# Kernel tuning notes

Measured on AMD Instinct MI355X. Metric: run time of the kernel, lower is better.

The kernel has to match this reference:

```python
import jax, jax.numpy as jnp
import numpy as np

NEG_SLOPE = 0.2


def setup_inputs() -> dict:
    key = jax.random.key(0)
    k1, k2, k3 = jax.random.split(key, 3)
    bs, n_agents, input_dim = 32, 512, 128
    n_heads, hidden_dim = 8, 64
    h = jax.random.normal(k1, (bs, n_agents, input_dim), dtype=jnp.float32)
    # Linear(input_dim, n_heads*hidden_dim, bias=False), stored as [in, out]
    W = jax.random.normal(k2, (input_dim, n_heads * hidden_dim), dtype=jnp.float32) * (1.0 / np.sqrt(input_dim))
    # xavier_uniform with gain=1.414 on shape (1, n_heads, 2*hidden_dim)
    fan = n_heads + 2 * hidden_dim
    bound = 1.414 * np.sqrt(6.0 / fan)
    att_a = jax.random.uniform(k3, (1, n_heads, 2 * hidden_dim), dtype=jnp.float32,
                               minval=-bound, maxval=bound)
    return {"h": h, "W": W, "att_a": att_a}


def reference(h, W, att_a):
    bs, n_agents, _ = h.shape
    n_heads = att_a.shape[1]
    hidden_dim = att_a.shape[2] // 2
    # h_prime: [bs, n_heads, n_agents, hidden_dim]
    h_prime = (h @ W).reshape(bs, n_agents, n_heads, hidden_dim).transpose(0, 2, 1, 3)
    # Additive score decomposes exactly: (a1.h_i + a2.h_j) == sum(cat(h_i,h_j)*a)
    a_src = att_a[0, :, :hidden_dim]   # [n_heads, hidden_dim]
    a_dst = att_a[0, :, hidden_dim:]   # [n_heads, hidden_dim]
    e_src = jnp.einsum('bhnd,hd->bhn', h_prime, a_src)  # score contribution of node i (row)
    e_dst = jnp.einsum('bhnd,hd->bhn', h_prime, a_dst)  # contribution of node j (col)
    e = e_src[:, :, :, None] + e_dst[:, :, None, :]     # [bs, n_heads, n, n]
    e = jnp.where(e >= 0, e, NEG_SLOPE * e)             # leaky_relu(0.2)
    attention = jax.nn.softmax(e, axis=-1)
    h_new = jnp.einsum('bhnm,bhmd->bhnd', attention, h_prime)
    return jax.nn.elu(h_new)
```

## Files before the change

kernel.cpp:

```cpp
#include <hip/hip_runtime.h>

#define BS 32
#define NA 512
#define ID 128
#define NH 8
#define HD 64
#define NHD 512
#define NEG 0.2f
#define NC 32
#define CH 16
#define NW 8

__global__ __launch_bounds__(256) void k1_gemm(
    const float* __restrict__ h, const float* __restrict__ W,
    float* __restrict__ hp) {
  int blk = blockIdx.x;
  int b = blk >> 5;
  int n0 = (blk & 31) * 16;
  int t = threadIdx.x;
  int lane = t & 63, w = t >> 6;
  int r0 = __builtin_amdgcn_readfirstlane((w >> 1) * 8);
  int chalf = __builtin_amdgcn_readfirstlane(w & 1);
  int col = chalf * 256 + lane * 4;
  int head = col >> 6;
  int d0 = col & 63;
  const float* arow = h + ((size_t)b * NA + n0 + r0) * ID;
  const float* wptr = W + col;

  float4 a0c = {0,0,0,0}, a1c = {0,0,0,0}, a2c = {0,0,0,0}, a3c = {0,0,0,0};
  float4 a4c = {0,0,0,0}, a5c = {0,0,0,0}, a6c = {0,0,0,0}, a7c = {0,0,0,0};

#define K1_ROW(I, C, KK)                                                      \
  { float a_ = arow[(I) * ID + kc + (KK)];                                    \
    C.x += a_ * wv.x; C.y += a_ * wv.y; C.z += a_ * wv.z; C.w += a_ * wv.w; }
  #pragma unroll 1
  for (int kc = 0; kc < ID; kc += 8) {
    #pragma unroll
    for (int kk = 0; kk < 8; ++kk) {
      float4 wv = *(const float4*)(wptr + (size_t)(kc + kk) * NHD);
      K1_ROW(0, a0c, kk) K1_ROW(1, a1c, kk) K1_ROW(2, a2c, kk)
      K1_ROW(3, a3c, kk) K1_ROW(4, a4c, kk) K1_ROW(5, a5c, kk)
      K1_ROW(6, a6c, kk) K1_ROW(7, a7c, kk)
    }
  }
#undef K1_ROW
  size_t off = ((((size_t)b * NH + head) * NA) + (n0 + r0)) * HD + d0;
  *(float4*)(hp + off) = a0c; off += HD;
  *(float4*)(hp + off) = a1c; off += HD;
  *(float4*)(hp + off) = a2c; off += HD;
  *(float4*)(hp + off) = a3c; off += HD;
  *(float4*)(hp + off) = a4c; off += HD;
  *(float4*)(hp + off) = a5c; off += HD;
  *(float4*)(hp + off) = a6c; off += HD;
  *(float4*)(hp + off) = a7c;
}

__global__ __launch_bounds__(512, 2) void k2_fused(
    const float* __restrict__ att, float* __restrict__ io) {
  __shared__ float tv[NA]; __shared__ int tpm[NA];
  __shared__ float sv[NA]; __shared__ int spm[NA];
  __shared__ float wp[NA]; __shared__ float wn[NA];
  __shared__ float rawP8[NW * 64]; __shared__ float rawN8[NW * 64];
  __shared__ float sufPc[(NW + 1) * 64]; __shared__ float preNc[(NW + 1) * 64];
  __shared__ float zps[NA + 1]; __shared__ float znp[NA + 1];
  __shared__ float szP[NC]; __shared__ float szN[NC];
  __shared__ float sufZ[NC + 1]; __shared__ float preZ[NC + 1];
  __shared__ float4 abi[NA];
  __shared__ int jsr[NA];
  __shared__ int Earr[NA];
  __shared__ float asrc[HD]; __shared__ float adst[HD];

  int bh = blockIdx.x;
  int head = bh & (NH - 1);
  int t = threadIdx.x;
  int lane = t & 63, w = t >> 6;
  float* vbase = io + (size_t)bh * NA * HD;

  if (t < 2 * HD) {
    float a = att[head * 2 * HD + t];
    if (t < HD) asrc[t] = a; else adst[t - HD] = a;
  }
  __syncthreads();

  float vt, vs; int it = t, is_ = t;
  {
    const float4* vr = (const float4*)(vbase + (size_t)t * HD);
    float s0 = 0.f, s1 = 0.f, t0 = 0.f, t1 = 0.f;
    #pragma unroll
    for (int j = 0; j < HD / 4; j += 2) {
      float4 v0 = vr[j], v1 = vr[j + 1];
      s0 += v0.x*asrc[4*j+0] + v0.y*asrc[4*j+1] + v0.z*asrc[4*j+2] + v0.w*asrc[4*j+3];
      t0 += v0.x*adst[4*j+0] + v0.y*adst[4*j+1] + v0.z*adst[4*j+2] + v0.w*adst[4*j+3];
      s1 += v1.x*asrc[4*j+4] + v1.y*asrc[4*j+5] + v1.z*asrc[4*j+6] + v1.w*asrc[4*j+7];
      t1 += v1.x*adst[4*j+4] + v1.y*adst[4*j+5] + v1.z*adst[4*j+6] + v1.w*adst[4*j+7];
    }
    vs = s0 + s1; vt = t0 + t1;
  }

  for (int size = 2; size <= NA; size <<= 1) {
    bool dirAsc = ((t & size) == 0);
    for (int stride = size >> 1; stride > 0; stride >>= 1) {
      float pt, ps; int pit, pis;
      if (stride >= 64) {
        tv[t] = vt; tpm[t] = it; sv[t] = vs; spm[t] = is_;
        __syncthreads();
        pt = tv[t ^ stride]; pit = tpm[t ^ stride];
        ps = sv[t ^ stride]; pis = spm[t ^ stride];
        __syncthreads();
      } else {
        pt = __shfl_xor(vt, stride, 64); pit = __shfl_xor(it, stride, 64);
        ps = __shfl_xor(vs, stride, 64); pis = __shfl_xor(is_, stride, 64);
      }
      bool mn = (((t & stride) == 0) == dirAsc);
      if (mn ? (pt < vt) : (pt > vt)) { vt = pt; it = pit; }
      if (mn ? (ps < vs) : (ps > vs)) { vs = ps; is_ = pis; }
    }
  }
  tv[t] = vt; tpm[t] = it; sv[t] = vs; spm[t] = is_;
  __syncthreads();

  float cmax = fmaxf(tv[NA - 1], 0.f);
  float amax = fmaxf(sv[NA - 1], 0.f);
  wp[t] = __expf(vt - cmax);
  wn[t] = __expf(NEG * vt - cmax);
  __syncthreads();

  float vreg[64];
  {
    float aP = 0.f, aN = 0.f;
    #pragma unroll
    for (int jj = 0; jj < 64; ++jj) {
      int j = (w << 6) + jj;
      float vv = vbase[(size_t)tpm[j] * HD + lane];
      vreg[jj] = vv;
      aP += wp[j] * vv;
      aN += wn[j] * vv;
    }
    rawP8[(w << 6) + lane] = aP;
    rawN8[(w << 6) + lane] = aN;
  }
  __syncthreads();

  if (t < 64) {
    int d = t; float run = 0.f;
    sufPc[NW * 64 + d] = 0.f;
    for (int ww = NW - 1; ww >= 0; --ww) {
      run += rawP8[ww * 64 + d]; sufPc[ww * 64 + d] = run;
    }
  } else if (t < 128) {
    int d = t - 64; float run = 0.f;
    for (int ww = 0; ww <= NW; ++ww) {
      preNc[ww * 64 + d] = run;
      if (ww < NW) run += rawN8[ww * 64 + d];
    }
  } else if (t < 160) {
    int c = t - 128; float a = 0.f;
    for (int j = c * CH; j < c * CH + CH; ++j) a += wp[j];
    szP[c] = a;
  } else if (t < 192) {
    int c = t - 160; float a = 0.f;
    for (int j = c * CH; j < c * CH + CH; ++j) a += wn[j];
    szN[c] = a;
  }
  __syncthreads();

  if (t == 0) {
    float run = 0.f; sufZ[NC] = 0.f;
    for (int cc = NC - 1; cc >= 0; --cc) { run += szP[cc]; sufZ[cc] = run; }
  } else if (t == 1) {
    float run = 0.f;
    for (int cc = 0; cc <= NC; ++cc) { preZ[cc] = run; if (cc < NC) run += szN[cc]; }
  }
  __syncthreads();

  {
    int ch = t >> 4;
    float a = 0.f;
    for (int k = t; k < ch * CH + CH; ++k) a += wp[k];
    zps[t] = a + sufZ[ch + 1];
    float b2 = 0.f;
    for (int k = ch * CH; k < t; ++k) b2 += wn[k];
    znp[t] = preZ[ch] + b2;
    if (t == 0) { zps[NA] = 0.f; znp[NA] = preZ[NC]; }
  }
  __syncthreads();

  {
    float A = __expf(vs - amax);
    float B = __expf(NEG * vs - amax);
    float key = -vs;
    int lo = 0, hi = NA;
    while (lo < hi) { int mid = (lo + hi) >> 1; if (tv[mid] < key) lo = mid + 1; else hi = mid; }
    float den = A * zps[lo] + B * znp[lo];
    float4 q; q.x = A; q.y = B; q.z = 1.f / den; q.w = __int_as_float(is_);
    abi[t] = q;
    jsr[t] = lo;
  }
  __syncthreads();

  {
    int lo = 0, hi = NA;
    while (lo < hi) { int mid = (lo + hi) >> 1; if (jsr[mid] > t) lo = mid + 1; else hi = mid; }
    Earr[t] = lo;
  }
  __syncthreads();

  {
    float sufPv = sufPc[w * 64 + lane];
    float preSeedN = preNc[w * 64 + lane];
    float runN = 0.f;
    size_t obase = (size_t)bh * NA * HD + lane;
    int eprev = (w == 0) ? NA : Earr[(w << 6) - 1];
    #pragma unroll
    for (int jj = 0; jj < 64; ++jj) {
      int j = (w << 6) + jj;
      int ecur = Earr[j];
      float preNv = preSeedN + runN;
      for (int r = ecur; r < eprev; ++r) {
        float4 q = abi[r];
        float x = (q.x * sufPv + q.y * preNv) * q.z;
        int orow = __float_as_int(q.w);
        io[obase + (size_t)orow * HD] = x > 0.f ? x : __expf(x) - 1.f;
      }
      float vv = vreg[jj];
      sufPv -= wp[j] * vv;
      runN  += wn[j] * vv;
      eprev = ecur;
    }
    if (w == NW - 1) {
      float preNv = preSeedN + runN;
      for (int r = 0; r < eprev; ++r) {
        float4 q = abi[r];
        float x = (q.y * preNv) * q.z;
        int orow = __float_as_int(q.w);
        io[obase + (size_t)orow * HD] = x > 0.f ? x : __expf(x) - 1.f;
      }
    }
  }
}

extern "C" void kernel_launch(void* const* d_in, const int* in_sizes, int n_in,
                              void* d_out, int out_size, void* d_ws, size_t ws_size,
                              hipStream_t stream) {
  const float* h   = (const float*)d_in[0];
  const float* W   = (const float*)d_in[1];
  const float* att = (const float*)d_in[2];
  float* io = (float*)d_out;
  (void)d_ws; (void)ws_size;

  k1_gemm <<<dim3(1024),    dim3(256), 0, stream>>>(h, W, io);
  k2_fused<<<dim3(BS * NH), dim3(512), 0, stream>>>(att, io);
}
```

Before: 134.9 us.

## Replace scalar FP32 projection GEMM with split-bf16 MFMA kernel

Rewrites the h@W projection kernel to use MFMA 16x16x32 bf16 instructions. FP32 inputs are split into hi and lo bf16 parts and three products are summed (hi*hi, hi*lo, lo*hi) to keep close to FP32 accuracy. W tiles are staged in padded LDS as bf16 and each block computes a 128x64 output tile for one head. This targets the ALU cost of the scalar FMA GEMM, at the cost of conversion work and a small loss of precision.

Measured after the change: 126.1 us. 6.5% less time.

```diff
diff --git a/kernel.cpp b/kernel.cpp
--- a/kernel.cpp
+++ b/kernel.cpp
@@ -10,49 +10,105 @@
 #define NC 32
 #define CH 16
 #define NW 8
-
-__global__ __launch_bounds__(256) void k1_gemm(
+#define BPAD 136
+
+typedef short bf16x8 __attribute__((ext_vector_type(8)));
+typedef float f32x4 __attribute__((ext_vector_type(4)));
+
+__device__ inline unsigned f2bf_bits(float x) {
+  unsigned u = __float_as_uint(x);
+  return (u + 0x7FFFu + ((u >> 16) & 1u)) >> 16;
+}
+
+__device__ inline void split8(const float4& x, const float4& y,
+                              bf16x8& hi, bf16x8& lo) {
+  float f[8] = {x.x, x.y, x.z, x.w, y.x, y.y, y.z, y.w};
+  #pragma unroll
+  for (int j = 0; j < 8; ++j) {
+    unsigned hb = f2bf_bits(f[j]);
+    float r = f[j] - __uint_as_float(hb << 16);
+    unsigned lb = f2bf_bits(r);
+    hi[j] = (short)hb;
+    lo[j] = (short)lb;
+  }
+}
+
+__global__ __launch_bounds__(256, 4) void k1_mfma(
     const float* __restrict__ h, const float* __restrict__ W,
-    float* __restrict__ hp) {
+    float* __restrict__ io) {
+  __shared__ unsigned short Bhi[64 * BPAD];
+  __shared__ unsigned short Blo[64 * BPAD];
+
   int blk = blockIdx.x;
-  int b = blk >> 5;
-  int n0 = (blk & 31) * 16;
+  int mt = blk >> 3;
+  int n0 = (blk & 7) * 64;
+  int m0 = mt * 128;
+  int b = mt >> 2;
+  int nbase = (mt & 3) * 128;
+  int head = n0 >> 6;
   int t = threadIdx.x;
   int lane = t & 63, w = t >> 6;
-  int r0 = __builtin_amdgcn_readfirstlane((w >> 1) * 8);
-  int chalf = __builtin_amdgcn_readfirstlane(w & 1);
-  int col = chalf * 256 + lane * 4;
-  int head = col >> 6;
-  int d0 = col & 63;
-  const float* arow = h + ((size_t)b * NA + n0 + r0) * ID;
-  const float* wptr = W + col;
-
-  float4 a0c = {0,0,0,0}, a1c = {0,0,0,0}, a2c = {0,0,0,0}, a3c = {0,0,0,0};
-  float4 a4c = {0,0,0,0}, a5c = {0,0,0,0}, a6c = {0,0,0,0}, a7c = {0,0,0,0};
-
-#define K1_ROW(I, C, KK)                                                      \
-  { float a_ = arow[(I) * ID + kc + (KK)];                                    \
-    C.x += a_ * wv.x; C.y += a_ * wv.y; C.z += a_ * wv.z; C.w += a_ * wv.w; }
-  #pragma unroll 1
-  for (int kc = 0; kc < ID; kc += 8) {
-    #pragma unroll
-    for (int kk = 0; kk < 8; ++kk) {
-      float4 wv = *(const float4*)(wptr + (size_t)(kc + kk) * NHD);
-      K1_ROW(0, a0c, kk) K1_ROW(1, a1c, kk) K1_ROW(2, a2c, kk)
-      K1_ROW(3, a3c, kk) K1_ROW(4, a4c, kk) K1_ROW(5, a5c, kk)
-      K1_ROW(6, a6c, kk) K1_ROW(7, a7c, kk)
-    }
-  }
-#undef K1_ROW
-  size_t off = ((((size_t)b * NH + head) * NA) + (n0 + r0)) * HD + d0;
-  *(float4*)(hp + off) = a0c; off += HD;
-  *(float4*)(hp + off) = a1c; off += HD;
-  *(float4*)(hp + off) = a2c; off += HD;
-  *(float4*)(hp + off) = a3c; off += HD;
-  *(float4*)(hp + off) = a4c; off += HD;
-  *(float4*)(hp + off) = a5c; off += HD;
-  *(float4*)(hp + off) = a6c; off += HD;
-  *(float4*)(hp + off) = a7c;
+  int q = lane >> 4, ml = lane & 15;
+
+  {
+    int c = t & 63, kq = t >> 6;
+    const float* wsrc = W + (size_t)kq * 32 * NHD + n0 + c;
+    #pragma unroll 4
+    for (int kk = 0; kk < 32; ++kk) {
+      int k = kq * 32 + kk;
+      float x = wsrc[(size_t)kk * NHD];
+      unsigned hb = f2bf_bits(x);
+      float r = x - __uint_as_float(hb << 16);
+      Bhi[c * BPAD + k] = (unsigned short)hb;
+      Blo[c * BPAD + k] = (unsigned short)f2bf_bits(r);
+    }
+  }
+  __syncthreads();
+
+  f32x4 acc[2][4];
+  #pragma unroll
+  for (int mf = 0; mf < 2; ++mf)
+    #pragma unroll
+    for (int nf = 0; nf < 4; ++nf)
+      acc[mf][nf] = (f32x4){0.f, 0.f, 0.f, 0.f};
+
+  const float* A0 = h + (size_t)(m0 + w * 32 + ml) * ID;
+
+  #pragma unroll
+  for (int ks = 0; ks < 4; ++ks) {
+    int ko = ks * 32 + q * 8;
+    bf16x8 ah[2], al[2];
+    #pragma unroll
+    for (int mf = 0; mf < 2; ++mf) {
+      const float* ap = A0 + mf * 16 * ID + ko;
+      float4 f0 = *(const float4*)ap;
+      float4 f1 = *(const float4*)(ap + 4);
+      split8(f0, f1, ah[mf], al[mf]);
+    }
+    #pragma unroll
+    for (int nf = 0; nf < 4; ++nf) {
+      int bo = (nf * 16 + ml) * BPAD + ko;
+      bf16x8 bh = *(const bf16x8*)&Bhi[bo];
+      bf16x8 bl = *(const bf16x8*)&Blo[bo];
+      #pragma unroll
+      for (int mf = 0; mf < 2; ++mf) {
+        acc[mf][nf] = __builtin_amdgcn_mfma_f32_16x16x32_bf16(ah[mf], bh, acc[mf][nf], 0, 0, 0);
+        acc[mf][nf] = __builtin_amdgcn_mfma_f32_16x16x32_bf16(ah[mf], bl, acc[mf][nf], 0, 0, 0);
+        acc[mf][nf] = __builtin_amdgcn_mfma_f32_16x16x32_bf16(al[mf], bh, acc[mf][nf], 0, 0, 0);
+      }
+    }
+  }
+
+  {
+    float* ob = io + (((size_t)b * NH + head) * NA + nbase + w * 32) * HD + ml;
+    #pragma unroll
+    for (int mf = 0; mf < 2; ++mf)
+      #pragma unroll
+      for (int nf = 0; nf < 4; ++nf)
+        #pragma unroll
+        for (int r = 0; r < 4; ++r)
+          ob[(size_t)(mf * 16 + q * 4 + r) * HD + nf * 16] = acc[mf][nf][r];
+  }
 }
 
 __global__ __launch_bounds__(512, 2) void k2_fused(
@@ -192,8 +248,8 @@
     int lo = 0, hi = NA;
     while (lo < hi) { int mid = (lo + hi) >> 1; if (tv[mid] < key) lo = mid + 1; else hi = mid; }
     float den = A * zps[lo] + B * znp[lo];
-    float4 q; q.x = A; q.y = B; q.z = 1.f / den; q.w = __int_as_float(is_);
-    abi[t] = q;
+    float4 qv; qv.x = A; qv.y = B; qv.z = 1.f / den; qv.w = __int_as_float(is_);
+    abi[t] = qv;
     jsr[t] = lo;
   }
   __syncthreads();
@@ -217,9 +273,9 @@
       int ecur = Earr[j];
       float preNv = preSeedN + runN;
       for (int r = ecur; r < eprev; ++r) {
-        float4 q = abi[r];
-        float x = (q.x * sufPv + q.y * preNv) * q.z;
-        int orow = __float_as_int(q.w);
+        float4 qv = abi[r];
+        float x = (qv.x * sufPv + qv.y * preNv) * qv.z;
+        int orow = __float_as_int(qv.w);
         io[obase + (size_t)orow * HD] = x > 0.f ? x : __expf(x) - 1.f;
       }
       float vv = vreg[jj];
@@ -230,9 +286,9 @@
     if (w == NW - 1) {
       float preNv = preSeedN + runN;
       for (int r = 0; r < eprev; ++r) {
-        float4 q = abi[r];
-        float x = (q.y * preNv) * q.z;
-        int orow = __float_as_int(q.w);
+        float4 qv = abi[r];
+        float x = (qv.y * preNv) * qv.z;
+        int orow = __float_as_int(qv.w);
         io[obase + (size_t)orow * HD] = x > 0.f ? x : __expf(x) - 1.f;
       }
     }
@@ -248,6 +304,6 @@
   float* io = (float*)d_out;
   (void)d_ws; (void)ws_size;
 
-  k1_gemm <<<dim3(1024),    dim3(256), 0, stream>>>(h, W, io);
+  k1_mfma <<<dim3(1024),    dim3(256), 0, stream>>>(h, W, io);
   k2_fused<<<dim3(BS * NH), dim3(512), 0, stream>>>(att, io);
 }
```
